# Optimization experiments

Measured on AMD Instinct MI355X. Metric: run time of the kernel, lower is better.

The kernel has to match this reference:

```python
import jax, jax.numpy as jnp
import numpy as np
import math

EMBED = 1024
HEADS = 16
HEAD_DIM = EMBED // HEADS


def setup_inputs() -> dict:
    key = jax.random.key(0)
    ks = jax.random.split(key, 9)
    B, S = 2, 2048
    query = jax.random.normal(ks[0], (B, S, EMBED), dtype=jnp.float32)
    key_t = jax.random.normal(ks[1], (B, S, EMBED), dtype=jnp.float32)
    value = jax.random.normal(ks[2], (B, S, EMBED), dtype=jnp.float32)
    mask = jax.random.randint(ks[3], (B, 1, S, S), 0, 2, dtype=jnp.int32)
    # nn.Linear(head_dim, head_dim, bias=False) weights: [out, in]
    sc = 1.0 / math.sqrt(HEAD_DIM)
    Wq = jax.random.uniform(ks[4], (HEAD_DIM, HEAD_DIM), jnp.float32, -sc, sc)
    Wk = jax.random.uniform(ks[5], (HEAD_DIM, HEAD_DIM), jnp.float32, -sc, sc)
    Wv = jax.random.uniform(ks[6], (HEAD_DIM, HEAD_DIM), jnp.float32, -sc, sc)
    so = 1.0 / math.sqrt(EMBED)
    Wo = jax.random.uniform(ks[7], (EMBED, EMBED), jnp.float32, -so, so)
    bo = jax.random.uniform(ks[8], (EMBED,), jnp.float32, -so, so)
    return {"query": query, "key": key_t, "value": value, "mask": mask,
            "Wq": Wq, "Wk": Wk, "Wv": Wv, "Wo": Wo, "bo": bo}


def reference(query, key, value, mask, Wq, Wk, Wv, Wo, bo):
    B, Sq, E = query.shape
    Sk = key.shape[1]
    H, D = HEADS, HEAD_DIM
    # Faithful raw reshape into heads (as in the torch source, no transpose)
    q = query.reshape(B, H, Sq, D)
    k = key.reshape(B, H, Sk, D)
    v = value.reshape(B, H, Sk, D)
    # per-head_dim Linear (bias-free): x @ W.T
    Q = jnp.einsum('bhsd,ed->bhse', q, Wq)
    K = jnp.einsum('bhsd,ed->bhse', k, Wk)
    V = jnp.einsum('bhsd,ed->bhse', v, Wv)
    scores = jnp.einsum('bhqd,bhkd->bhqk', Q, K)  # [B,H,Sq,Sk]
    scores = jnp.where(mask == 0, jnp.float32(-1e20), scores)
    # NOTE: source divides by sqrt(embed_size), not sqrt(head_dim)
    attn = jax.nn.softmax(scores / jnp.float32(math.sqrt(E)), axis=-1)
    out = jnp.einsum('bhqk,bhkd->bhqd', attn, V).reshape(B, Sq, H * D)
    return out @ Wo.T + bo
```

## Files before the change

kernel.cpp:

```cpp
#include <hip/hip_runtime.h>

typedef __attribute__((ext_vector_type(8))) short short8;
typedef __attribute__((ext_vector_type(4))) float f32x4;
typedef __attribute__((ext_vector_type(2))) int int2v;

__device__ __forceinline__ short f2bf(float f) {
  unsigned u = __builtin_bit_cast(unsigned, f);
  u += 0x7fff + ((u >> 16) & 1);
  return (short)(u >> 16);
}

__device__ __forceinline__ int pk2bf(float lo, float hi) {
#if defined(__gfx950__) && __has_builtin(__builtin_amdgcn_cvt_pk_bf16_f32)
  typedef __attribute__((ext_vector_type(2))) __bf16 bf16x2;
  bf16x2 v = __builtin_amdgcn_cvt_pk_bf16_f32(lo, hi);
  return __builtin_bit_cast(int, v);
#else
  return (int)(unsigned short)(short)f2bf(lo) | (((int)f2bf(hi)) << 16);
#endif
}

__device__ __forceinline__ float fand(float p, int m) {
  return __builtin_bit_cast(float, __builtin_bit_cast(int, p) & m);
}

__device__ __forceinline__ int bmask(unsigned nib, int bit) {
#if __has_builtin(__builtin_amdgcn_sbfe)
  return __builtin_amdgcn_sbfe((int)nib, bit, 1);
#else
  return -(int)((nib >> bit) & 1);
#endif
}

__device__ __forceinline__ float fexp2(float x) {
#if __has_builtin(__builtin_amdgcn_exp2f)
  return __builtin_amdgcn_exp2f(x);
#else
  return exp2f(x);
#endif
}

__global__ __launch_bounds__(256) void cvtall(const float* __restrict__ Wo,
                                              const float* __restrict__ Wq,
                                              const float* __restrict__ Wk,
                                              const float* __restrict__ Wv,
                                              short* __restrict__ Wob,
                                              short* __restrict__ Wqb,
                                              short* __restrict__ Wkb,
                                              short* __restrict__ Wvb) {
  int bid = blockIdx.x;
  const float* s;
  short* d;
  int base;
  if (bid < 1024) { s = Wo; d = Wob; base = bid; }
  else if (bid < 1028) { s = Wq; d = Wqb; base = bid - 1024; }
  else if (bid < 1032) { s = Wk; d = Wkb; base = bid - 1028; }
  else { s = Wv; d = Wvb; base = bid - 1032; }
  int i = (base * 256 + threadIdx.x) * 4;
#pragma unroll
  for (int j = 0; j < 4; ++j) d[i + j] = f2bf(s[i + j]);
}

__global__ __launch_bounds__(256) void packmask(const int* __restrict__ mask,
                                                unsigned long long* __restrict__ mpk) {
  int gid = blockIdx.x * 256 + threadIdx.x;
  int base = gid & ~63;
  int j = gid & 63;
  int v = mask[base + ((j & 3) << 4) + (j >> 2)];
  unsigned long long bal = __ballot(v != 0);
  if (j == 0) mpk[gid >> 6] = bal;
}

__global__ __launch_bounds__(256) void projall(const float* __restrict__ q,
                                               const float* __restrict__ k,
                                               const float* __restrict__ v,
                                               const short* __restrict__ Wqb,
                                               const short* __restrict__ Wkb,
                                               const short* __restrict__ Wvb,
                                               short* __restrict__ Qp,
                                               short* __restrict__ Kp,
                                               short* __restrict__ Vtp) {
  __shared__ short xt[64][72];
  __shared__ short ot[64][72];
  const int mode = blockIdx.x >> 10;
  const int bid = blockIdx.x & 1023;
  const float* X;
  const short* Wb;
  short* Out;
  float scale;
  if (mode == 0) { X = q; Wb = Wqb; Out = Qp; scale = 0.045084220f; }
  else if (mode == 1) { X = k; Wb = Wkb; Out = Kp; scale = 1.0f; }
  else { X = v; Wb = Wvb; Out = Vtp; scale = 1.0f; }

  const int tid = threadIdx.x;
  const int r0 = bid * 64;
  const int row = tid >> 2, seg = (tid & 3) << 4;

  const float* src = X + (r0 + row) * 64 + seg;
  short8 v0, v1;
#pragma unroll
  for (int i = 0; i < 8; ++i) { v0[i] = f2bf(src[i]); v1[i] = f2bf(src[8 + i]); }
  *(short8*)&xt[row][seg] = v0;
  *(short8*)&xt[row][seg + 8] = v1;
  __syncthreads();

  const int lane = tid & 63, wave = tid >> 6;
  const int m16 = lane & 15, quad = lane >> 4;

  short8 a0 = *(const short8*)&xt[wave * 16 + m16][quad * 8];
  short8 a1 = *(const short8*)&xt[wave * 16 + m16][32 + quad * 8];

  f32x4 acc[4];
#pragma unroll
  for (int nt = 0; nt < 4; ++nt) {
    short8 b0 = *(const short8*)&Wb[(nt * 16 + m16) * 64 + quad * 8];
    short8 b1 = *(const short8*)&Wb[(nt * 16 + m16) * 64 + 32 + quad * 8];
    f32x4 z = (f32x4){0.f, 0.f, 0.f, 0.f};
    z = __builtin_amdgcn_mfma_f32_16x16x32_bf16(a0, b0, z, 0, 0, 0);
    z = __builtin_amdgcn_mfma_f32_16x16x32_bf16(a1, b1, z, 0, 0, 0);
    acc[nt] = z;
  }

  if (mode != 2) {
#pragma unroll
    for (int nt = 0; nt < 4; ++nt)
#pragma unroll
      for (int r = 0; r < 4; ++r)
        Out[(r0 + wave * 16 + quad * 4 + r) * 64 + nt * 16 + m16] = f2bf(acc[nt][r] * scale);
  } else {
#pragma unroll
    for (int nt = 0; nt < 4; ++nt)
#pragma unroll
      for (int r = 0; r < 4; ++r)
        ot[wave * 16 + quad * 4 + r][nt * 16 + m16] = f2bf(acc[nt][r]);
    __syncthreads();
    const int bh = r0 >> 11, s0 = r0 & 2047;
    const int d = tid >> 2, c4 = tid & 3;
    short* ob = Out + bh * 131072 + d * 2048 + s0 + c4;
#pragma unroll
    for (int i = 0; i < 16; ++i) ob[4 * i] = ot[c4 * 16 + i][d];
  }
}

__global__ __launch_bounds__(256) void flash64(const short* __restrict__ Qp,
                                               const short* __restrict__ Kp,
                                               const short* __restrict__ Vt,
                                               const unsigned long long* __restrict__ mpk,
                                               short* __restrict__ O) {
  __shared__ short kt[64][72];
  __shared__ short vt[64][72];
  __shared__ __attribute__((aligned(16))) short pt[64][72];
  const int tid = threadIdx.x;
  const int bid = blockIdx.x;
  const int bh = bid >> 5, qt = bid & 31;
  const int b = bh >> 4;
  const int q0 = qt << 6;
  const short* Qh = Qp + bh * 131072;
  const short* Kh = Kp + bh * 131072;
  const short* Vh = Vt + bh * 131072;
  const int lane = tid & 63, wave = tid >> 6;
  const int m16 = lane & 15, quad = lane >> 4;
  const int row = tid >> 2, seg = (tid & 3) << 4;
  const int prow = wave * 16 + quad * 4;
  const unsigned long long* mrow = mpk + (b * 2048 + q0 + prow) * 32;
  const int msh = m16 * 4;

  const short8 aq0 = *(const short8*)&Qh[(q0 + wave * 16 + m16) * 64 + quad * 8];
  const short8 aq1 = *(const short8*)&Qh[(q0 + wave * 16 + m16) * 64 + 32 + quad * 8];

  float lrow[4] = {0.f, 0.f, 0.f, 0.f};
  f32x4 oacc[4];
#pragma unroll
  for (int d = 0; d < 4; ++d) oacc[d] = (f32x4){0.f, 0.f, 0.f, 0.f};

  for (int kti = 0; kti < 32; ++kti) {
    const int k0 = kti << 6;
    __syncthreads();
    *(short8*)&kt[row][seg] = *(const short8*)&Kh[(k0 + row) * 64 + seg];
    *(short8*)&kt[row][seg + 8] = *(const short8*)&Kh[(k0 + row) * 64 + seg + 8];
    *(short8*)&vt[row][seg] = *(const short8*)&Vh[row * 2048 + k0 + seg];
    *(short8*)&vt[row][seg + 8] = *(const short8*)&Vh[row * 2048 + k0 + seg + 8];
    __syncthreads();

    f32x4 s[4];
#pragma unroll
    for (int nt = 0; nt < 4; ++nt) {
      short8 b0 = *(const short8*)&kt[nt * 16 + m16][quad * 8];
      short8 b1 = *(const short8*)&kt[nt * 16 + m16][32 + quad * 8];
      f32x4 z = (f32x4){0.f, 0.f, 0.f, 0.f};
      z = __builtin_amdgcn_mfma_f32_16x16x32_bf16(aq0, b0, z, 0, 0, 0);
      z = __builtin_amdgcn_mfma_f32_16x16x32_bf16(aq1, b1, z, 0, 0, 0);
      s[nt] = z;
    }

    unsigned nib[4];
#pragma unroll
    for (int r = 0; r < 4; ++r) {
      unsigned long long w = mrow[r * 32 + kti];
      nib[r] = (unsigned)(w >> msh) & 15u;
    }

#pragma unroll
    for (int r = 0; r < 4; ++r) {
      float p0 = fand(fexp2(s[0][r]), bmask(nib[r], 0));
      float p1 = fand(fexp2(s[1][r]), bmask(nib[r], 1));
      float p2 = fand(fexp2(s[2][r]), bmask(nib[r], 2));
      float p3 = fand(fexp2(s[3][r]), bmask(nib[r], 3));
      lrow[r] += (p0 + p1) + (p2 + p3);
      int2v pp;
      pp.x = pk2bf(p0, p1);
      pp.y = pk2bf(p2, p3);
      *(int2v*)&pt[prow + r][msh] = pp;
    }

    short8 ap0 = *(const short8*)&pt[wave * 16 + m16][quad * 8];
    short8 ap1 = *(const short8*)&pt[wave * 16 + m16][32 + quad * 8];
#pragma unroll
    for (int dt = 0; dt < 4; ++dt) {
      short8 b0 = *(const short8*)&vt[dt * 16 + m16][quad * 8];
      short8 b1 = *(const short8*)&vt[dt * 16 + m16][32 + quad * 8];
      f32x4 z = oacc[dt];
      z = __builtin_amdgcn_mfma_f32_16x16x32_bf16(ap0, b0, z, 0, 0, 0);
      z = __builtin_amdgcn_mfma_f32_16x16x32_bf16(ap1, b1, z, 0, 0, 0);
      oacc[dt] = z;
    }
  }

#pragma unroll
  for (int r = 0; r < 4; ++r) {
#pragma unroll
    for (int off = 1; off < 16; off <<= 1) lrow[r] += __shfl_xor(lrow[r], off, 16);
  }

#pragma unroll
  for (int r = 0; r < 4; ++r) {
    float inv = 1.0f / lrow[r];
#pragma unroll
    for (int dt = 0; dt < 4; ++dt)
      O[(bh * 2048 + q0 + wave * 16 + quad * 4 + r) * 64 + dt * 16 + m16] =
          f2bf(oacc[dt][r] * inv);
  }
}

__global__ __launch_bounds__(256) void outproj(const short* __restrict__ Ob,
                                               const short* __restrict__ Wob,
                                               const float* __restrict__ bo,
                                               float* __restrict__ out) {
  __shared__ short at[128][72];
  __shared__ short bt[128][72];
  const int tid = threadIdx.x;
  const int bid = blockIdx.x;
  const int ct = bid & 7, rt = bid >> 3;
  const int r0 = rt * 128, c0 = ct * 128;
  const int lane = tid & 63, wave = tid >> 6;
  const int wr = (wave >> 1) * 64, wc = (wave & 1) * 64;
  const int m16 = lane & 15, quad = lane >> 4;
  const int srow = tid >> 1, shalf = (tid & 1) * 32;

  f32x4 acc[4][4];
#pragma unroll
  for (int mt = 0; mt < 4; ++mt)
#pragma unroll
    for (int nt = 0; nt < 4; ++nt) acc[mt][nt] = (f32x4){0.f, 0.f, 0.f, 0.f};

  for (int kc = 0; kc < 16; ++kc) {
    __syncthreads();
    const short* ag = &Ob[(r0 + srow) * 1024 + kc * 64 + shalf];
    const short* bg = &Wob[(c0 + srow) * 1024 + kc * 64 + shalf];
    *(short8*)&at[srow][shalf] = *(const short8*)&ag[0];
    *(short8*)&at[srow][shalf + 8] = *(const short8*)&ag[8];
    *(short8*)&at[srow][shalf + 16] = *(const short8*)&ag[16];
    *(short8*)&at[srow][shalf + 24] = *(const short8*)&ag[24];
    *(short8*)&bt[srow][shalf] = *(const short8*)&bg[0];
    *(short8*)&bt[srow][shalf + 8] = *(const short8*)&bg[8];
    *(short8*)&bt[srow][shalf + 16] = *(const short8*)&bg[16];
    *(short8*)&bt[srow][shalf + 24] = *(const short8*)&bg[24];
    __syncthreads();

#pragma unroll
    for (int kh = 0; kh < 2; ++kh) {
      short8 af[4], bf[4];
#pragma unroll
      for (int i = 0; i < 4; ++i) {
        af[i] = *(const short8*)&at[wr + i * 16 + m16][kh * 32 + quad * 8];
        bf[i] = *(const short8*)&bt[wc + i * 16 + m16][kh * 32 + quad * 8];
      }
#pragma unroll
      for (int mt = 0; mt < 4; ++mt)
#pragma unroll
        for (int nt = 0; nt < 4; ++nt)
          acc[mt][nt] = __builtin_amdgcn_mfma_f32_16x16x32_bf16(af[mt], bf[nt], acc[mt][nt], 0, 0, 0);
    }
  }

#pragma unroll
  for (int nt = 0; nt < 4; ++nt) {
    const int col = c0 + wc + nt * 16 + m16;
    const float bias = bo[col];
#pragma unroll
    for (int mt = 0; mt < 4; ++mt)
#pragma unroll
      for (int rr = 0; rr < 4; ++rr)
        out[(r0 + wr + mt * 16 + quad * 4 + rr) * 1024 + col] = acc[mt][nt][rr] + bias;
  }
}

extern "C" void kernel_launch(void* const* d_in, const int* in_sizes, int n_in,
                              void* d_out, int out_size, void* d_ws, size_t ws_size,
                              hipStream_t stream) {
  const float* query = (const float*)d_in[0];
  const float* key = (const float*)d_in[1];
  const float* value = (const float*)d_in[2];
  const int* mask = (const int*)d_in[3];
  const float* Wq = (const float*)d_in[4];
  const float* Wk = (const float*)d_in[5];
  const float* Wv = (const float*)d_in[6];
  const float* Wo = (const float*)d_in[7];
  const float* bo = (const float*)d_in[8];
  float* out = (float*)d_out;

  char* ws = (char*)d_ws;
  short* Qp = (short*)(ws);
  short* Kp = (short*)(ws + 8388608);
  short* Vt = (short*)(ws + 16777216);
  short* Ob = (short*)(ws + 25165824);
  short* Wob = (short*)(ws + 33554432);
  short* Wqb = (short*)(ws + 35651584);
  short* Wkb = (short*)(ws + 35659776);
  short* Wvb = (short*)(ws + 35667968);
  unsigned long long* mpk = (unsigned long long*)(ws + 35676160);

  cvtall<<<1036, 256, 0, stream>>>(Wo, Wq, Wk, Wv, Wob, Wqb, Wkb, Wvb);
  packmask<<<32768, 256, 0, stream>>>(mask, mpk);
  projall<<<3072, 256, 0, stream>>>(query, key, value, Wqb, Wkb, Wvb, Qp, Kp, Vt);
  flash64<<<1024, 256, 0, stream>>>(Qp, Kp, Vt, mpk, Ob);
  outproj<<<256, 256, 0, stream>>>(Ob, Wob, bo, out);
}
```

Before: 246.9 us.

## Fuse prep kernels and widen flash attention to 128-row query tiles

Merges weight conversion, mask packing and Q/K/V projection into a single prep launch, with vectorized float4 loads and coalesced stores staged through LDS. Per-head weights are now converted to bf16 inside the projection blocks. The attention kernel processes 128 query rows per block, reusing each K/V tile across two 16-row groups per wave. K/V tiles are loaded straight into LDS with global_load_lds into an XOR-swizzled layout, and the block-to-head mapping is remapped. The aim is fewer launches and less LDS and global traffic per unit of work, at the cost of higher register pressure and only 512 attention blocks.

```diff
diff --git a/kernel.cpp b/kernel.cpp
--- a/kernel.cpp
+++ b/kernel.cpp
@@ -3,6 +3,7 @@
 typedef __attribute__((ext_vector_type(8))) short short8;
 typedef __attribute__((ext_vector_type(4))) float f32x4;
 typedef __attribute__((ext_vector_type(2))) int int2v;
+typedef __attribute__((ext_vector_type(4))) int int4v;
 
 __device__ __forceinline__ short f2bf(float f) {
   unsigned u = __builtin_bit_cast(unsigned, f);
@@ -20,6 +21,15 @@
 #endif
 }
 
+__device__ __forceinline__ short8 pack8(f32x4 a, f32x4 b) {
+  int4v t;
+  t.x = pk2bf(a[0], a[1]);
+  t.y = pk2bf(a[2], a[3]);
+  t.z = pk2bf(b[0], b[1]);
+  t.w = pk2bf(b[2], b[3]);
+  return __builtin_bit_cast(short8, t);
+}
+
 __device__ __forceinline__ float fand(float p, int m) {
   return __builtin_bit_cast(float, __builtin_bit_cast(int, p) & m);
 }
@@ -40,81 +50,85 @@
 #endif
 }
 
-__global__ __launch_bounds__(256) void cvtall(const float* __restrict__ Wo,
-                                              const float* __restrict__ Wq,
-                                              const float* __restrict__ Wk,
-                                              const float* __restrict__ Wv,
-                                              short* __restrict__ Wob,
-                                              short* __restrict__ Wqb,
-                                              short* __restrict__ Wkb,
-                                              short* __restrict__ Wvb) {
-  int bid = blockIdx.x;
-  const float* s;
-  short* d;
-  int base;
-  if (bid < 1024) { s = Wo; d = Wob; base = bid; }
-  else if (bid < 1028) { s = Wq; d = Wqb; base = bid - 1024; }
-  else if (bid < 1032) { s = Wk; d = Wkb; base = bid - 1028; }
-  else { s = Wv; d = Wvb; base = bid - 1032; }
-  int i = (base * 256 + threadIdx.x) * 4;
-#pragma unroll
-  for (int j = 0; j < 4; ++j) d[i + j] = f2bf(s[i + j]);
-}
-
-__global__ __launch_bounds__(256) void packmask(const int* __restrict__ mask,
-                                                unsigned long long* __restrict__ mpk) {
-  int gid = blockIdx.x * 256 + threadIdx.x;
-  int base = gid & ~63;
-  int j = gid & 63;
-  int v = mask[base + ((j & 3) << 4) + (j >> 2)];
-  unsigned long long bal = __ballot(v != 0);
-  if (j == 0) mpk[gid >> 6] = bal;
-}
-
-__global__ __launch_bounds__(256) void projall(const float* __restrict__ q,
-                                               const float* __restrict__ k,
-                                               const float* __restrict__ v,
-                                               const short* __restrict__ Wqb,
-                                               const short* __restrict__ Wkb,
-                                               const short* __restrict__ Wvb,
-                                               short* __restrict__ Qp,
-                                               short* __restrict__ Kp,
-                                               short* __restrict__ Vtp) {
+__device__ __forceinline__ void glds16(const short* g, short* lbase, int lane) {
+#if __has_builtin(__builtin_amdgcn_global_load_lds)
+  __builtin_amdgcn_global_load_lds(
+      (const __attribute__((address_space(1))) unsigned int*)g,
+      (__attribute__((address_space(3))) unsigned int*)lbase, 16, 0, 0);
+#else
+  *(short8*)(lbase + lane * 8) = *(const short8*)g;
+#endif
+}
+
+__global__ __launch_bounds__(256) void prep(const float* __restrict__ q,
+                                            const float* __restrict__ k,
+                                            const float* __restrict__ v,
+                                            const float* __restrict__ Wq,
+                                            const float* __restrict__ Wk,
+                                            const float* __restrict__ Wv,
+                                            const float* __restrict__ Wo,
+                                            const int* __restrict__ mask,
+                                            short* __restrict__ Qp,
+                                            short* __restrict__ Kp,
+                                            short* __restrict__ Vtp,
+                                            short* __restrict__ Wob,
+                                            unsigned long long* __restrict__ mpk) {
+  const int bid = blockIdx.x;
+  const int tid = threadIdx.x;
+
+  if (bid >= 4096) {
+#pragma unroll
+    for (int it = 0; it < 4; ++it) {
+      const int gid = ((bid - 4096) * 4 + it) * 256 + tid;
+      const int base = gid & ~63, j = gid & 63;
+      const int val = mask[base + ((j & 3) << 4) + (j >> 2)];
+      const unsigned long long bal = __ballot(val != 0);
+      if (j == 0) mpk[gid >> 6] = bal;
+    }
+    return;
+  }
+  if (bid >= 3072) {
+    const int i = ((bid - 3072) * 256 + tid) * 4;
+    const f32x4 x = *(const f32x4*)&Wo[i];
+    int2v o;
+    o.x = pk2bf(x[0], x[1]);
+    o.y = pk2bf(x[2], x[3]);
+    *(int2v*)&Wob[i] = o;
+    return;
+  }
+
   __shared__ short xt[64][72];
   __shared__ short ot[64][72];
-  const int mode = blockIdx.x >> 10;
-  const int bid = blockIdx.x & 1023;
+  const int mode = bid >> 10;
+  const int bt = bid & 1023;
   const float* X;
-  const short* Wb;
-  short* Out;
+  const float* W;
   float scale;
-  if (mode == 0) { X = q; Wb = Wqb; Out = Qp; scale = 0.045084220f; }
-  else if (mode == 1) { X = k; Wb = Wkb; Out = Kp; scale = 1.0f; }
-  else { X = v; Wb = Wvb; Out = Vtp; scale = 1.0f; }
-
-  const int tid = threadIdx.x;
-  const int r0 = bid * 64;
-  const int row = tid >> 2, seg = (tid & 3) << 4;
-
-  const float* src = X + (r0 + row) * 64 + seg;
-  short8 v0, v1;
-#pragma unroll
-  for (int i = 0; i < 8; ++i) { v0[i] = f2bf(src[i]); v1[i] = f2bf(src[8 + i]); }
-  *(short8*)&xt[row][seg] = v0;
-  *(short8*)&xt[row][seg + 8] = v1;
+  if (mode == 0) { X = q; W = Wq; scale = 0.045084220f; }
+  else if (mode == 1) { X = k; W = Wk; scale = 1.0f; }
+  else { X = v; W = Wv; scale = 1.0f; }
+
+  const int r0 = bt * 64;
+  const int row = tid >> 2, seg = (tid & 3) * 16;
+  const f32x4* xs = (const f32x4*)(X + (r0 + row) * 64 + seg);
+  const f32x4 x0 = xs[0], x1 = xs[1], x2 = xs[2], x3 = xs[3];
+  *(short8*)&xt[row][seg] = pack8(x0, x1);
+  *(short8*)&xt[row][seg + 8] = pack8(x2, x3);
   __syncthreads();
 
   const int lane = tid & 63, wave = tid >> 6;
   const int m16 = lane & 15, quad = lane >> 4;
 
-  short8 a0 = *(const short8*)&xt[wave * 16 + m16][quad * 8];
-  short8 a1 = *(const short8*)&xt[wave * 16 + m16][32 + quad * 8];
+  const short8 a0 = *(const short8*)&xt[wave * 16 + m16][quad * 8];
+  const short8 a1 = *(const short8*)&xt[wave * 16 + m16][32 + quad * 8];
 
   f32x4 acc[4];
 #pragma unroll
   for (int nt = 0; nt < 4; ++nt) {
-    short8 b0 = *(const short8*)&Wb[(nt * 16 + m16) * 64 + quad * 8];
-    short8 b1 = *(const short8*)&Wb[(nt * 16 + m16) * 64 + 32 + quad * 8];
+    const f32x4* wp0 = (const f32x4*)&W[(nt * 16 + m16) * 64 + quad * 8];
+    const f32x4* wp1 = (const f32x4*)&W[(nt * 16 + m16) * 64 + 32 + quad * 8];
+    const short8 b0 = pack8(wp0[0], wp0[1]);
+    const short8 b1 = pack8(wp1[0], wp1[1]);
     f32x4 z = (f32x4){0.f, 0.f, 0.f, 0.f};
     z = __builtin_amdgcn_mfma_f32_16x16x32_bf16(a0, b0, z, 0, 0, 0);
     z = __builtin_amdgcn_mfma_f32_16x16x32_bf16(a1, b1, z, 0, 0, 0);
@@ -126,120 +140,157 @@
     for (int nt = 0; nt < 4; ++nt)
 #pragma unroll
       for (int r = 0; r < 4; ++r)
-        Out[(r0 + wave * 16 + quad * 4 + r) * 64 + nt * 16 + m16] = f2bf(acc[nt][r] * scale);
+        ot[wave * 16 + quad * 4 + r][nt * 16 + m16] = f2bf(acc[nt][r] * scale);
   } else {
 #pragma unroll
     for (int nt = 0; nt < 4; ++nt)
 #pragma unroll
       for (int r = 0; r < 4; ++r)
-        ot[wave * 16 + quad * 4 + r][nt * 16 + m16] = f2bf(acc[nt][r]);
-    __syncthreads();
+        ot[nt * 16 + m16][16 * quad + 4 * r + wave] = f2bf(acc[nt][r]);
+  }
+  __syncthreads();
+
+  const int orow = tid >> 2, opart = tid & 3;
+  if (mode != 2) {
+    short* dst = (mode == 0 ? Qp : Kp) + (r0 + orow) * 64 + opart * 16;
+    *(short8*)&dst[0] = *(const short8*)&ot[orow][opart * 16];
+    *(short8*)&dst[8] = *(const short8*)&ot[orow][opart * 16 + 8];
+  } else {
     const int bh = r0 >> 11, s0 = r0 & 2047;
-    const int d = tid >> 2, c4 = tid & 3;
-    short* ob = Out + bh * 131072 + d * 2048 + s0 + c4;
-#pragma unroll
-    for (int i = 0; i < 16; ++i) ob[4 * i] = ot[c4 * 16 + i][d];
-  }
-}
-
-__global__ __launch_bounds__(256) void flash64(const short* __restrict__ Qp,
-                                               const short* __restrict__ Kp,
-                                               const short* __restrict__ Vt,
-                                               const unsigned long long* __restrict__ mpk,
-                                               short* __restrict__ O) {
-  __shared__ short kt[64][72];
-  __shared__ short vt[64][72];
-  __shared__ __attribute__((aligned(16))) short pt[64][72];
+    short* dst = Vtp + bh * 131072 + orow * 2048 + s0 + opart * 16;
+    *(short8*)&dst[0] = *(const short8*)&ot[orow][opart * 16];
+    *(short8*)&dst[8] = *(const short8*)&ot[orow][opart * 16 + 8];
+  }
+}
+
+__global__ __launch_bounds__(256) void flash128(const short* __restrict__ Qp,
+                                                const short* __restrict__ Kp,
+                                                const short* __restrict__ Vt,
+                                                const unsigned long long* __restrict__ mpk,
+                                                short* __restrict__ O) {
+  __shared__ __attribute__((aligned(16))) short kt[4096];
+  __shared__ __attribute__((aligned(16))) short vt[4096];
+  __shared__ __attribute__((aligned(16))) short pt[128][72];
   const int tid = threadIdx.x;
   const int bid = blockIdx.x;
-  const int bh = bid >> 5, qt = bid & 31;
+  const int local = bid >> 3;
+  const int bh = (bid & 7) * 4 + (local >> 4);
+  const int q0 = (local & 15) << 7;
   const int b = bh >> 4;
-  const int q0 = qt << 6;
   const short* Qh = Qp + bh * 131072;
   const short* Kh = Kp + bh * 131072;
   const short* Vh = Vt + bh * 131072;
   const int lane = tid & 63, wave = tid >> 6;
   const int m16 = lane & 15, quad = lane >> 4;
-  const int row = tid >> 2, seg = (tid & 3) << 4;
-  const int prow = wave * 16 + quad * 4;
-  const unsigned long long* mrow = mpk + (b * 2048 + q0 + prow) * 32;
+  const int srow = lane >> 3, sj = (lane & 7) ^ srow;
   const int msh = m16 * 4;
-
-  const short8 aq0 = *(const short8*)&Qh[(q0 + wave * 16 + m16) * 64 + quad * 8];
-  const short8 aq1 = *(const short8*)&Qh[(q0 + wave * 16 + m16) * 64 + 32 + quad * 8];
-
-  float lrow[4] = {0.f, 0.f, 0.f, 0.f};
-  f32x4 oacc[4];
-#pragma unroll
-  for (int d = 0; d < 4; ++d) oacc[d] = (f32x4){0.f, 0.f, 0.f, 0.f};
+  const int koff = m16 * 128 + ((quad ^ (m16 & 7)) * 16);
+
+  short8 aq[2][2];
+#pragma unroll
+  for (int g = 0; g < 2; ++g)
+#pragma unroll
+    for (int h = 0; h < 2; ++h)
+      aq[g][h] = *(const short8*)&Qh[(q0 + wave * 32 + g * 16 + m16) * 64 + h * 32 + quad * 8];
+
+  const unsigned long long* mq = mpk + (b * 2048 + q0 + wave * 32 + quad * 4) * 32;
+
+  float l[2][4];
+  f32x4 oacc[2][4];
+#pragma unroll
+  for (int g = 0; g < 2; ++g)
+#pragma unroll
+    for (int r = 0; r < 4; ++r) l[g][r] = 0.f;
+#pragma unroll
+  for (int g = 0; g < 2; ++g)
+#pragma unroll
+    for (int dt = 0; dt < 4; ++dt) oacc[g][dt] = (f32x4){0.f, 0.f, 0.f, 0.f};
 
   for (int kti = 0; kti < 32; ++kti) {
     const int k0 = kti << 6;
     __syncthreads();
-    *(short8*)&kt[row][seg] = *(const short8*)&Kh[(k0 + row) * 64 + seg];
-    *(short8*)&kt[row][seg + 8] = *(const short8*)&Kh[(k0 + row) * 64 + seg + 8];
-    *(short8*)&vt[row][seg] = *(const short8*)&Vh[row * 2048 + k0 + seg];
-    *(short8*)&vt[row][seg + 8] = *(const short8*)&Vh[row * 2048 + k0 + seg + 8];
+#pragma unroll
+    for (int t = 0; t < 2; ++t) {
+      const int crow = wave * 16 + t * 8;
+      const int grow = crow + srow;
+      glds16(Kh + (k0 + grow) * 64 + sj * 8, kt + crow * 64, lane);
+      glds16(Vh + grow * 2048 + k0 + sj * 8, vt + crow * 64, lane);
+    }
     __syncthreads();
 
-    f32x4 s[4];
+    f32x4 s[2][4];
 #pragma unroll
     for (int nt = 0; nt < 4; ++nt) {
-      short8 b0 = *(const short8*)&kt[nt * 16 + m16][quad * 8];
-      short8 b1 = *(const short8*)&kt[nt * 16 + m16][32 + quad * 8];
-      f32x4 z = (f32x4){0.f, 0.f, 0.f, 0.f};
-      z = __builtin_amdgcn_mfma_f32_16x16x32_bf16(aq0, b0, z, 0, 0, 0);
-      z = __builtin_amdgcn_mfma_f32_16x16x32_bf16(aq1, b1, z, 0, 0, 0);
-      s[nt] = z;
-    }
-
-    unsigned nib[4];
+      const int o0 = nt * 2048 + koff;
+      const short8 kb0 = *(const short8*)((const char*)kt + o0);
+      const short8 kb1 = *(const short8*)((const char*)kt + (o0 ^ 64));
+#pragma unroll
+      for (int g = 0; g < 2; ++g) {
+        f32x4 z = (f32x4){0.f, 0.f, 0.f, 0.f};
+        z = __builtin_amdgcn_mfma_f32_16x16x32_bf16(aq[g][0], kb0, z, 0, 0, 0);
+        z = __builtin_amdgcn_mfma_f32_16x16x32_bf16(aq[g][1], kb1, z, 0, 0, 0);
+        s[g][nt] = z;
+      }
+    }
+
+#pragma unroll
+    for (int g = 0; g < 2; ++g) {
+#pragma unroll
+      for (int r = 0; r < 4; ++r) {
+        const unsigned long long w = mq[g * 512 + r * 32 + kti];
+        const unsigned nib = (unsigned)(w >> msh) & 15u;
+        const float p0 = fand(fexp2(s[g][0][r]), bmask(nib, 0));
+        const float p1 = fand(fexp2(s[g][1][r]), bmask(nib, 1));
+        const float p2 = fand(fexp2(s[g][2][r]), bmask(nib, 2));
+        const float p3 = fand(fexp2(s[g][3][r]), bmask(nib, 3));
+        l[g][r] += (p0 + p1) + (p2 + p3);
+        int2v pp;
+        pp.x = pk2bf(p0, p1);
+        pp.y = pk2bf(p2, p3);
+        *(int2v*)&pt[wave * 32 + g * 16 + quad * 4 + r][msh] = pp;
+      }
+    }
+
+    short8 ap[2][2];
+#pragma unroll
+    for (int g = 0; g < 2; ++g)
+#pragma unroll
+      for (int h = 0; h < 2; ++h)
+        ap[g][h] = *(const short8*)&pt[wave * 32 + g * 16 + m16][h * 32 + quad * 8];
+
+#pragma unroll
+    for (int dt = 0; dt < 4; ++dt) {
+      const int o0 = dt * 2048 + koff;
+      const short8 vb0 = *(const short8*)((const char*)vt + o0);
+      const short8 vb1 = *(const short8*)((const char*)vt + (o0 ^ 64));
+#pragma unroll
+      for (int g = 0; g < 2; ++g) {
+        f32x4 z = oacc[g][dt];
+        z = __builtin_amdgcn_mfma_f32_16x16x32_bf16(ap[g][0], vb0, z, 0, 0, 0);
+        z = __builtin_amdgcn_mfma_f32_16x16x32_bf16(ap[g][1], vb1, z, 0, 0, 0);
+        oacc[g][dt] = z;
+      }
+    }
+  }
+
+#pragma unroll
+  for (int g = 0; g < 2; ++g)
 #pragma unroll
     for (int r = 0; r < 4; ++r) {
-      unsigned long long w = mrow[r * 32 + kti];
-      nib[r] = (unsigned)(w >> msh) & 15u;
-    }
-
-#pragma unroll
-    for (int r = 0; r < 4; ++r) {
-      float p0 = fand(fexp2(s[0][r]), bmask(nib[r], 0));
-      float p1 = fand(fexp2(s[1][r]), bmask(nib[r], 1));
-      float p2 = fand(fexp2(s[2][r]), bmask(nib[r], 2));
-      float p3 = fand(fexp2(s[3][r]), bmask(nib[r], 3));
-      lrow[r] += (p0 + p1) + (p2 + p3);
-      int2v pp;
-      pp.x = pk2bf(p0, p1);
-      pp.y = pk2bf(p2, p3);
-      *(int2v*)&pt[prow + r][msh] = pp;
-    }
-
-    short8 ap0 = *(const short8*)&pt[wave * 16 + m16][quad * 8];
-    short8 ap1 = *(const short8*)&pt[wave * 16 + m16][32 + quad * 8];
-#pragma unroll
-    for (int dt = 0; dt < 4; ++dt) {
-      short8 b0 = *(const short8*)&vt[dt * 16 + m16][quad * 8];
-      short8 b1 = *(const short8*)&vt[dt * 16 + m16][32 + quad * 8];
-      f32x4 z = oacc[dt];
-      z = __builtin_amdgcn_mfma_f32_16x16x32_bf16(ap0, b0, z, 0, 0, 0);
-      z = __builtin_amdgcn_mfma_f32_16x16x32_bf16(ap1, b1, z, 0, 0, 0);
-      oacc[dt] = z;
-    }
-  }
-
-#pragma unroll
-  for (int r = 0; r < 4; ++r) {
-#pragma unroll
-    for (int off = 1; off < 16; off <<= 1) lrow[r] += __shfl_xor(lrow[r], off, 16);
-  }
-
-#pragma unroll
-  for (int r = 0; r < 4; ++r) {
-    float inv = 1.0f / lrow[r];
-#pragma unroll
-    for (int dt = 0; dt < 4; ++dt)
-      O[(bh * 2048 + q0 + wave * 16 + quad * 4 + r) * 64 + dt * 16 + m16] =
-          f2bf(oacc[dt][r] * inv);
-  }
+#pragma unroll
+      for (int off = 1; off < 16; off <<= 1) l[g][r] += __shfl_xor(l[g][r], off, 16);
+      const float inv = 1.0f / l[g][r];
+#pragma unroll
+      for (int dt = 0; dt < 4; ++dt)
+        pt[wave * 32 + g * 16 + quad * 4 + r][dt * 16 + m16] = f2bf(oacc[g][dt][r] * inv);
+    }
+
+  const int orow = lane >> 1, opart = lane & 1;
+  const int prow = wave * 32 + orow;
+  short* og = O + (bh * 2048 + q0 + prow) * 64 + opart * 32;
+#pragma unroll
+  for (int c = 0; c < 32; c += 8)
+    *(short8*)&og[c] = *(const short8*)&pt[prow][opart * 32 + c];
 }
 
 __global__ __launch_bounds__(256) void outproj(const short* __restrict__ Ob,
@@ -325,14 +376,10 @@
   short* Vt = (short*)(ws + 16777216);
   short* Ob = (short*)(ws + 25165824);
   short* Wob = (short*)(ws + 33554432);
-  short* Wqb = (short*)(ws + 35651584);
-  short* Wkb = (short*)(ws + 35659776);
-  short* Wvb = (short*)(ws + 35667968);
-  unsigned long long* mpk = (unsigned long long*)(ws + 35676160);
-
-  cvtall<<<1036, 256, 0, stream>>>(Wo, Wq, Wk, Wv, Wob, Wqb, Wkb, Wvb);
-  packmask<<<32768, 256, 0, stream>>>(mask, mpk);
-  projall<<<3072, 256, 0, stream>>>(query, key, value, Wqb, Wkb, Wvb, Qp, Kp, Vt);
-  flash64<<<1024, 256, 0, stream>>>(Qp, Kp, Vt, mpk, Ob);
+  unsigned long long* mpk = (unsigned long long*)(ws + 35651584);
+
+  prep<<<12288, 256, 0, stream>>>(query, key, value, Wq, Wk, Wv, Wo, mask,
+                                  Qp, Kp, Vt, Wob, mpk);
+  flash128<<<512, 256, 0, stream>>>(Qp, Kp, Vt, mpk, Ob);
   outproj<<<256, 256, 0, stream>>>(Ob, Wob, bo, out);
 }
```

After: 261.7 us. 6.0% more time.
